# Kernel tuning notes

Hardware: AMD Instinct MI355X
Metric: run time of the kernel (lower is better)

The kernel has to match this reference:

```python
import jax, jax.numpy as jnp
import numpy as np

B, LAT, HID = 256, 20, 128
G, BIN = 25000, 25       # original_dim, bin_size
C = 7                    # max_cp + 1 copy-number states
GB = G // BIN            # rho head output dim


def setup_inputs() -> dict:
    key = jax.random.key(0)
    ks = jax.random.split(key, 16)
    s = 0.01  # TruncatedNormal(stddev=0.01) init
    return {
        "z": jax.random.normal(ks[0], (B, LAT), jnp.float32),
        "w0": jax.random.normal(ks[1], (LAT, HID), jnp.float32) * s,
        "b0": jnp.zeros((HID,), jnp.float32),
        "g0": jnp.ones((HID,), jnp.float32),
        "be0": jnp.zeros((HID,), jnp.float32),
        "m0": jax.random.normal(ks[2], (HID,), jnp.float32) * 0.1,
        "v0": jax.random.uniform(ks[3], (HID,), jnp.float32, 0.5, 1.5),
        "w1": jax.random.normal(ks[4], (HID, HID), jnp.float32) * s,
        "b1": jnp.zeros((HID,), jnp.float32),
        "g1": jnp.ones((HID,), jnp.float32),
        "be1": jnp.zeros((HID,), jnp.float32),
        "m1": jax.random.normal(ks[5], (HID,), jnp.float32) * 0.1,
        "v1": jax.random.uniform(ks[6], (HID,), jnp.float32, 0.5, 1.5),
        "wr": jax.random.normal(ks[7], (HID, G), jnp.float32) * s,
        "br": jnp.zeros((G,), jnp.float32),
        "wd": jax.random.normal(ks[8], (HID, G), jnp.float32) * s,
        "bd": jnp.zeros((G,), jnp.float32),
        "wrho": jax.random.normal(ks[9], (C, HID, GB), jnp.float32) * s,
        "brho": jnp.zeros((C, GB), jnp.float32),
        "ws": jax.random.normal(ks[10], (G,), jnp.float32) * 0.05,
        "bs": jax.random.normal(ks[11], (G,), jnp.float32) * 0.05,
    }


def reference(z, w0, b0, g0, be0, m0, v0, w1, b1, g1, be1, m1, v1,
              wr, br, wd, bd, wrho, brho, ws, bs):
    BN_EPS = 1e-3
    EPS = 1e-20
    TEMP = 0.1

    def bn(x, gamma, beta, mean, var):
        # inference-mode BatchNormalization(momentum=0.01, epsilon=0.001)
        return (x - mean) * jax.lax.rsqrt(var + BN_EPS) * gamma + beta

    # FullyConnLayer x2: Dense -> BN -> ReLU
    x = jax.nn.relu(bn(z @ w0 + b0, g0, be0, m0, v0))
    x = jax.nn.relu(bn(x @ w1 + b1, g1, be1, m1, v1))

    theta = jnp.exp(x @ wr + br)        # [B, G]
    pi_drop = x @ wd + bd               # [B, G]

    # max_cp+1 rho Dense heads fused into a single batched GEMM -> [C, B, GB]
    rho = jnp.einsum('bh,cho->cbo', x, wrho) + brho[:, None, :]
    rho = jax.nn.softmax(rho, axis=0)   # softmax over copy-number states

    # GumbelSoftmaxSampling: stack(axis=1) -> [B, C, GB]
    rho_b = jnp.transpose(rho, (1, 0, 2))
    gene_rho = jnp.repeat(rho_b, BIN, axis=-1)        # [B, C, G]
    pi = jnp.transpose(gene_rho, (0, 2, 1))           # [B, G, C]

    u = jax.random.uniform(jax.random.key(42), pi.shape, jnp.float32)
    gnoise = -jnp.log(-jnp.log(u + EPS) + EPS)
    y = jax.nn.softmax((jnp.log(pi + EPS) + gnoise) / TEMP, axis=-1)
    y_hard = (y == jnp.max(y, axis=-1, keepdims=True)).astype(jnp.float32)
    y = jax.lax.stop_gradient(y_hard - y) + y         # straight-through

    # multiply by copy-number index matrix and reduce -> expected/sampled copy
    cvals = jnp.arange(C, dtype=jnp.float32)
    sample = jnp.sum(y * cvals, axis=-1)              # [B, G]

    # ScaleLayer: sigmoid(x * w + b)
    mu = jax.nn.sigmoid(sample * ws + bs)             # [B, G]
    return (mu, theta, pi_drop, sample, pi)
```

## Files before the change

### kernel.cpp

```cpp
#include <hip/hip_runtime.h>

#define B 256
#define LAT 20
#define HID 128
#define G 25000
#define GB 1000
#define NC 7

typedef __attribute__((ext_vector_type(8))) short short8;
typedef __attribute__((ext_vector_type(4))) float f32x4;

__device__ __forceinline__ unsigned short f2bf(float f) {
  unsigned int u = __float_as_uint(f);
  u += 0x7fffu + ((u >> 16) & 1u);
  return (unsigned short)(u >> 16);
}

__device__ __forceinline__ unsigned int threefry_xor(unsigned int idx) {
  unsigned int x0 = 0u;
  unsigned int x1 = idx + 42u;
#define TF_R(r) { x0 += x1; x1 = (x1 << r) | (x1 >> (32 - r)); x1 ^= x0; }
  TF_R(13) TF_R(15) TF_R(26) TF_R(6)
  x0 += 42u;          x1 += 0x1BD11BF1u;
  TF_R(17) TF_R(29) TF_R(16) TF_R(24)
  x0 += 0x1BD11BF0u;  x1 += 2u;
  TF_R(13) TF_R(15) TF_R(26) TF_R(6)
   x1 += 45u;
  TF_R(17) TF_R(29) TF_R(16) TF_R(24)
  x0 += 42u;          x1 += 0x1BD11BF4u;
  TF_R(13) TF_R(15) TF_R(26) TF_R(6)
  x0 += 0x1BD11BF0u;  x1 += 5u;
#undef TF_R
  return x0 ^ x1;
}

__global__ void k_mlp(const float* __restrict__ z,  const float* __restrict__ w0,
                      const float* __restrict__ b0, const float* __restrict__ g0,
                      const float* __restrict__ be0, const float* __restrict__ m0,
                      const float* __restrict__ v0,
                      const float* __restrict__ w1, const float* __restrict__ b1,
                      const float* __restrict__ g1, const float* __restrict__ be1,
                      const float* __restrict__ m1, const float* __restrict__ v1,
                      double* __restrict__ x64, unsigned short* __restrict__ x_bf) {
  __shared__ double xs[HID];
  const int b = blockIdx.x, h = threadIdx.x;
  double acc = (double)b0[h];
  for (int k = 0; k < LAT; ++k)
    acc += (double)z[b * LAT + k] * (double)w0[k * HID + h];
  double y = (acc - (double)m0[h]) * (1.0 / sqrt((double)v0[h] + 1e-3)) * (double)g0[h]
             + (double)be0[h];
  y = y > 0.0 ? y : 0.0;
  xs[h] = y;
  __syncthreads();
  double a1 = (double)b1[h];
  for (int k = 0; k < HID; ++k)
    a1 += xs[k] * (double)w1[k * HID + h];
  double y1 = (a1 - (double)m1[h]) * (1.0 / sqrt((double)v1[h] + 1e-3)) * (double)g1[h]
              + (double)be1[h];
  y1 = y1 > 0.0 ? y1 : 0.0;
  x64[h * B + b] = y1;
  x_bf[b * HID + h] = f2bf((float)y1);
}

__global__ void k_trans(const float* __restrict__ wr, const float* __restrict__ wd,
                        unsigned short* __restrict__ wrT, unsigned short* __restrict__ wdT) {
  __shared__ float t[64][65];
  const float* src = blockIdx.z ? wd : wr;
  unsigned short* dst = blockIdx.z ? wdT : wrT;
  const int g0 = blockIdx.x * 64, h0 = blockIdx.y * 64;
#pragma unroll
  for (int i = 0; i < 16; ++i) {
    int f = i * 256 + threadIdx.x;
    int hl = f >> 6, gl = f & 63;
    int g = g0 + gl;
    t[hl][gl] = (g < G) ? src[(h0 + hl) * G + g] : 0.f;
  }
  __syncthreads();
#pragma unroll
  for (int i = 0; i < 16; ++i) {
    int f = i * 256 + threadIdx.x;
    int gl = f >> 6, hl = f & 63;
    int g = g0 + gl;
    if (g < G) dst[(size_t)g * HID + h0 + hl] = f2bf(t[hl][gl]);
  }
}

__global__ __launch_bounds__(256) void k_rho(const double* __restrict__ x64,
                      const float* __restrict__ wrho, const float* __restrict__ brho,
                      float* __restrict__ pi32, float* __restrict__ lp32,
                      double* __restrict__ lp64) {
  __shared__ float wl[NC * HID * 4];
  const int o0 = blockIdx.x * 4, bB = blockIdx.y * 64;
  for (int i = threadIdx.x; i < NC * HID * 4; i += 256) {
    int ol = i & 3, rest = i >> 2;
    int c = rest >> 7, h = rest & 127;
    wl[i] = wrho[(c * HID + h) * GB + o0 + ol];
  }
  __syncthreads();
  const int lane = threadIdx.x & 63, ol = threadIdx.x >> 6;
  const int b = bB + lane, o = o0 + ol;
  double acc[NC];
#pragma unroll
  for (int c = 0; c < NC; ++c) acc[c] = (double)brho[c * GB + o];
  for (int h = 0; h < HID; ++h) {
    double xv = x64[h * B + b];
#pragma unroll
    for (int c = 0; c < NC; ++c)
      acc[c] += xv * (double)wl[(c * HID + h) * 4 + ol];
  }
  double m = acc[0];
#pragma unroll
  for (int c = 1; c < NC; ++c) m = fmax(m, acc[c]);
  double e[NC], s = 0.0;
#pragma unroll
  for (int c = 0; c < NC; ++c) { e[c] = exp(acc[c] - m); s += e[c]; }
  const size_t base = (size_t)o * (NC * B) + b;
#pragma unroll
  for (int c = 0; c < NC; ++c) {
    double pi = e[c] / s;
    double lp = log(pi + 1e-20);
    pi32[base + c * B] = (float)pi;
    lp32[base + c * B] = (float)lp;
    lp64[base + c * B] = lp;
  }
}

__global__ __launch_bounds__(256) void k_main(
    const unsigned short* __restrict__ x_bf,
    const unsigned short* __restrict__ wrT, const unsigned short* __restrict__ wdT,
    const float* __restrict__ br, const float* __restrict__ bd,
    const float* __restrict__ wsc, const float* __restrict__ bsc,
    const float* __restrict__ pi32, const float* __restrict__ lp32,
    const double* __restrict__ lp64, float* __restrict__ out) {
  __shared__ float s_lp[3 * NC * 128];
  __shared__ float s_pi[3 * NC * 128];
  const int tid = threadIdx.x;
  const int o_base = (blockIdx.x * 32) / 25;
  const int bB = blockIdx.y * 128;

  for (int i = tid; i < 3 * NC * 128; i += 256) {
    int ol = i / (NC * 128);
    int r = i - ol * (NC * 128);
    int c = r >> 7, bl = r & 127;
    int oo = o_base + ol; if (oo > GB - 1) oo = GB - 1;
    size_t src = (size_t)oo * (NC * B) + c * B + bB + bl;
    s_lp[i] = lp32[src];
    s_pi[i] = pi32[src];
  }

  const int wv = tid >> 6, lane = tid & 63;
  const int n = lane & 15, quad = lane >> 4;
  const int gt = wv & 1;
  const int btbase = blockIdx.y * 8 + (wv >> 1) * 4;
  const int g = blockIdx.x * 32 + gt * 16 + n;
  const bool gvalid = g < G;
  const int gcl = gvalid ? g : G - 1;
  const float brv = br[gcl], bdv = bd[gcl], wsv = wsc[gcl], bsv = bsc[gcl];
  const int o = gcl / 25;
  const int o_local = o - o_base;
  const double* lqb = lp64 + (size_t)o * (NC * B);

  short8 fr[4], fd[4];
  {
    const short8* p1 = (const short8*)(wrT + (size_t)gcl * HID + quad * 8);
    const short8* p2 = (const short8*)(wdT + (size_t)gcl * HID + quad * 8);
#pragma unroll
    for (int ks = 0; ks < 4; ++ks) { fr[ks] = p1[ks * 4]; fd[ks] = p2[ks * 4]; }
  }
  __syncthreads();

  for (int bti = 0; bti < 4; ++bti) {
    const int bt = btbase + bti;
    const short8* xp = (const short8*)(x_bf + (size_t)(bt * 16 + n) * HID + quad * 8);
    f32x4 accr = {0.f, 0.f, 0.f, 0.f}, accd = {0.f, 0.f, 0.f, 0.f};
#pragma unroll
    for (int ks = 0; ks < 4; ++ks) {
      short8 fa = xp[ks * 4];
      accr = __builtin_amdgcn_mfma_f32_16x16x32_bf16(fa, fr[ks], accr, 0, 0, 0);
      accd = __builtin_amdgcn_mfma_f32_16x16x32_bf16(fa, fd[ks], accd, 0, 0, 0);
    }
#pragma unroll
    for (int i = 0; i < 4; ++i) {
      const int b = bt * 16 + quad * 4 + i;
      const int b_local = (wv >> 1) * 64 + bti * 16 + quad * 4 + i;
      const float th = __expf(accr[i] + brv);
      const float pd = accd[i] + bdv;
      const float* lpp = s_lp + o_local * (NC * 128) + b_local;
      unsigned int bits[NC];
      const unsigned int idx0 = (unsigned int)b * 175000u + (unsigned int)g * 7u;
      float best = -3.4e38f, sec = -3.4e38f; int arg = 0;
#pragma unroll
      for (int c = 0; c < NC; ++c) {
        unsigned int bb = threefry_xor(idx0 + (unsigned int)c);
        bits[c] = bb;
        float uf = __uint_as_float((bb >> 9) | 0x3f800000u) - 1.0f;
        float v1m = 1.0f - uf;
        float ln_nat = -__logf(uf + 1e-20f);
        float ln_ser = v1m * (1.0f + v1m * (0.5f + 0.33333334f * v1m));
        float l1 = (v1m < 0.001953125f) ? ln_ser : ln_nat;
        float gn = -__logf(l1);
        float mv = lpp[c * 128] + gn;
        if (mv > best) { sec = best; best = mv; arg = c; }
        else if (mv > sec) sec = mv;
      }
      int s = arg;
      if (best - sec < 3e-4f) {
        double lv[NC], bestd = -1e300;
#pragma unroll
        for (int c = 0; c < NC; ++c) {
          float uf = __uint_as_float((bits[c] >> 9) | 0x3f800000u) - 1.0f;
          double gn = -log(-log((double)uf + 1e-20) + 1e-20);
          lv[c] = lqb[c * B + b] + gn;
          bestd = fmax(bestd, lv[c]);
        }
        s = 0;
#pragma unroll
        for (int c = 0; c < NC; ++c) if (lv[c] == bestd) s += c;
      }
      if (gvalid) {
        const float smp = (float)s;
        const float mu = __builtin_amdgcn_rcpf(1.f + __expf(-(smp * wsv + bsv)));
        const size_t og = (size_t)b * G + g;
        out[og] = mu;
        out[6400000 + og] = th;
        out[12800000 + og] = pd;
        out[19200000 + og] = smp;
        const float* pip = s_pi + o_local * (NC * 128) + b_local;
        const size_t pbo = 25600000 + og * 7;
#pragma unroll
        for (int c = 0; c < NC; ++c) out[pbo + c] = pip[c * 128];
      }
    }
  }
}

extern "C" void kernel_launch(void* const* d_in, const int* in_sizes, int n_in,
                              void* d_out, int out_size, void* d_ws, size_t ws_size,
                              hipStream_t stream) {
  const float* z   = (const float*)d_in[0];
  const float* w0  = (const float*)d_in[1];
  const float* b0  = (const float*)d_in[2];
  const float* g0  = (const float*)d_in[3];
  const float* be0 = (const float*)d_in[4];
  const float* m0  = (const float*)d_in[5];
  const float* v0  = (const float*)d_in[6];
  const float* w1  = (const float*)d_in[7];
  const float* b1  = (const float*)d_in[8];
  const float* g1  = (const float*)d_in[9];
  const float* be1 = (const float*)d_in[10];
  const float* m1  = (const float*)d_in[11];
  const float* v1  = (const float*)d_in[12];
  const float* wr  = (const float*)d_in[13];
  const float* br  = (const float*)d_in[14];
  const float* wd  = (const float*)d_in[15];
  const float* bd  = (const float*)d_in[16];
  const float* wrho= (const float*)d_in[17];
  const float* brho= (const float*)d_in[18];
  const float* wsc = (const float*)d_in[19];
  const float* bsc = (const float*)d_in[20];

  char* ws = (char*)d_ws;
  unsigned short* x_bf = (unsigned short*)(ws);
  double* x64          = (double*)(ws + 65536);
  unsigned short* wrT  = (unsigned short*)(ws + 327680);
  unsigned short* wdT  = (unsigned short*)(ws + 6727680);
  float* pi32          = (float*)(ws + 13127680);
  float* lp32          = (float*)(ws + 20295680);
  double* lp64         = (double*)(ws + 27463680);
  float* out = (float*)d_out;

  k_mlp<<<dim3(256), dim3(128), 0, stream>>>(z, w0, b0, g0, be0, m0, v0,
                                             w1, b1, g1, be1, m1, v1, x64, x_bf);
  k_trans<<<dim3(391, 2, 2), dim3(256), 0, stream>>>(wr, wd, wrT, wdT);
  k_rho<<<dim3(250, 4), dim3(256), 0, stream>>>(x64, wrho, brho, pi32, lp32, lp64);
  k_main<<<dim3(782, 2), dim3(256), 0, stream>>>(x_bf, wrT, wdT, br, bd, wsc, bsc,
                                                 pi32, lp32, lp64, out);
}
```

Before: 522.3 us.

## Defer near-tie double-precision Gumbel argmax fixups to a separate compacted kernel

Near-tie samples are no longer recomputed in double precision inside the main kernel. The main kernel appends their (b,g) indices to a global list via an atomic counter, and a small follow-up kernel recomputes and overwrites mu and sample for those entries. This removes divergent fp64 work and register pressure (bits array, unrolled loop) from the hot kernel. It also vectorizes the pi stores. In exchange it adds atomics, an extra launch, and a capped list that could overflow.

```diff
diff --git a/kernel.cpp b/kernel.cpp
--- a/kernel.cpp
+++ b/kernel.cpp
@@ -6,9 +6,12 @@
 #define G 25000
 #define GB 1000
 #define NC 7
+#define FIXCAP (1u << 20)
 
 typedef __attribute__((ext_vector_type(8))) short short8;
 typedef __attribute__((ext_vector_type(4))) float f32x4;
+typedef float v4fa __attribute__((vector_size(16), aligned(4)));
+typedef float v2fa __attribute__((vector_size(8), aligned(4)));
 
 __device__ __forceinline__ unsigned short f2bf(float f) {
   unsigned int u = __float_as_uint(f);
@@ -41,7 +44,10 @@
                       const float* __restrict__ w1, const float* __restrict__ b1,
                       const float* __restrict__ g1, const float* __restrict__ be1,
                       const float* __restrict__ m1, const float* __restrict__ v1,
-                      double* __restrict__ x64, unsigned short* __restrict__ x_bf) {
+                      double* __restrict__ x64, unsigned short* __restrict__ x_bf,
+                      unsigned int* __restrict__ fix_cnt) {
+  if (blockIdx.x == 0 && threadIdx.x == 0)
+    __hip_atomic_store(fix_cnt, 0u, __ATOMIC_RELAXED, __HIP_MEMORY_SCOPE_AGENT);
   __shared__ double xs[HID];
   const int b = blockIdx.x, h = threadIdx.x;
   double acc = (double)b0[h];
@@ -131,7 +137,8 @@
     const float* __restrict__ br, const float* __restrict__ bd,
     const float* __restrict__ wsc, const float* __restrict__ bsc,
     const float* __restrict__ pi32, const float* __restrict__ lp32,
-    const double* __restrict__ lp64, float* __restrict__ out) {
+    unsigned int* __restrict__ fix_cnt, unsigned int* __restrict__ fix_list,
+    float* __restrict__ out) {
   __shared__ float s_lp[3 * NC * 128];
   __shared__ float s_pi[3 * NC * 128];
   const int tid = threadIdx.x;
@@ -158,7 +165,6 @@
   const float brv = br[gcl], bdv = bd[gcl], wsv = wsc[gcl], bsv = bsc[gcl];
   const int o = gcl / 25;
   const int o_local = o - o_base;
-  const double* lqb = lp64 + (size_t)o * (NC * B);
 
   short8 fr[4], fd[4];
   {
@@ -186,13 +192,11 @@
       const float th = __expf(accr[i] + brv);
       const float pd = accd[i] + bdv;
       const float* lpp = s_lp + o_local * (NC * 128) + b_local;
-      unsigned int bits[NC];
       const unsigned int idx0 = (unsigned int)b * 175000u + (unsigned int)g * 7u;
       float best = -3.4e38f, sec = -3.4e38f; int arg = 0;
-#pragma unroll
+#pragma unroll 1
       for (int c = 0; c < NC; ++c) {
         unsigned int bb = threefry_xor(idx0 + (unsigned int)c);
-        bits[c] = bb;
         float uf = __uint_as_float((bb >> 9) | 0x3f800000u) - 1.0f;
         float v1m = 1.0f - uf;
         float ln_nat = -__logf(uf + 1e-20f);
@@ -200,25 +204,17 @@
         float l1 = (v1m < 0.001953125f) ? ln_ser : ln_nat;
         float gn = -__logf(l1);
         float mv = lpp[c * 128] + gn;
-        if (mv > best) { sec = best; best = mv; arg = c; }
-        else if (mv > sec) sec = mv;
-      }
-      int s = arg;
-      if (best - sec < 3e-4f) {
-        double lv[NC], bestd = -1e300;
-#pragma unroll
-        for (int c = 0; c < NC; ++c) {
-          float uf = __uint_as_float((bits[c] >> 9) | 0x3f800000u) - 1.0f;
-          double gn = -log(-log((double)uf + 1e-20) + 1e-20);
-          lv[c] = lqb[c * B + b] + gn;
-          bestd = fmax(bestd, lv[c]);
-        }
-        s = 0;
-#pragma unroll
-        for (int c = 0; c < NC; ++c) if (lv[c] == bestd) s += c;
+        bool gtb = mv > best;
+        sec = gtb ? best : (mv > sec ? mv : sec);
+        best = gtb ? mv : best;
+        arg = gtb ? c : arg;
       }
       if (gvalid) {
-        const float smp = (float)s;
+        if (best - sec < 3e-4f) {
+          unsigned int idx = atomicAdd(fix_cnt, 1u);
+          if (idx < FIXCAP) fix_list[idx] = ((unsigned int)b << 15) | (unsigned int)g;
+        }
+        const float smp = (float)arg;
         const float mu = __builtin_amdgcn_rcpf(1.f + __expf(-(smp * wsv + bsv)));
         const size_t og = (size_t)b * G + g;
         out[og] = mu;
@@ -227,10 +223,46 @@
         out[19200000 + og] = smp;
         const float* pip = s_pi + o_local * (NC * 128) + b_local;
         const size_t pbo = 25600000 + og * 7;
-#pragma unroll
-        for (int c = 0; c < NC; ++c) out[pbo + c] = pip[c * 128];
+        v4fa p4 = {pip[0], pip[128], pip[256], pip[384]};
+        v2fa p2 = {pip[512], pip[640]};
+        *(v4fa*)(out + pbo) = p4;
+        *(v2fa*)(out + pbo + 4) = p2;
+        out[pbo + 6] = pip[768];
       }
     }
+  }
+}
+
+__global__ void k_fix(const double* __restrict__ lp64,
+                      const float* __restrict__ wsc, const float* __restrict__ bsc,
+                      const unsigned int* __restrict__ fix_cnt,
+                      const unsigned int* __restrict__ fix_list,
+                      float* __restrict__ out) {
+  unsigned int nn = fix_cnt[0];
+  if (nn > FIXCAP) nn = FIXCAP;
+  for (unsigned int i = blockIdx.x * 256 + threadIdx.x; i < nn; i += gridDim.x * 256) {
+    unsigned int bg = fix_list[i];
+    int b = bg >> 15, g = bg & 32767;
+    int o = g / 25;
+    const double* lq = lp64 + (size_t)o * (NC * B) + b;
+    const unsigned int idx0 = (unsigned int)b * 175000u + (unsigned int)g * 7u;
+    double lv[NC], bestd = -1e300;
+#pragma unroll
+    for (int c = 0; c < NC; ++c) {
+      unsigned int bb = threefry_xor(idx0 + (unsigned int)c);
+      float uf = __uint_as_float((bb >> 9) | 0x3f800000u) - 1.0f;
+      double gn = -log(-log((double)uf + 1e-20) + 1e-20);
+      lv[c] = lq[c * B] + gn;
+      bestd = fmax(bestd, lv[c]);
+    }
+    int s = 0;
+#pragma unroll
+    for (int c = 0; c < NC; ++c) if (lv[c] == bestd) s += c;
+    const float smp = (float)s;
+    const float mu = __builtin_amdgcn_rcpf(1.f + __expf(-(smp * wsc[g] + bsc[g])));
+    const size_t og = (size_t)b * G + g;
+    out[og] = mu;
+    out[19200000 + og] = smp;
   }
 }
 
@@ -267,12 +299,15 @@
   float* pi32          = (float*)(ws + 13127680);
   float* lp32          = (float*)(ws + 20295680);
   double* lp64         = (double*)(ws + 27463680);
+  unsigned int* fix_cnt  = (unsigned int*)(ws + 48 * 1024 * 1024);
+  unsigned int* fix_list = (unsigned int*)(ws + 48 * 1024 * 1024 + 16);
   float* out = (float*)d_out;
 
   k_mlp<<<dim3(256), dim3(128), 0, stream>>>(z, w0, b0, g0, be0, m0, v0,
-                                             w1, b1, g1, be1, m1, v1, x64, x_bf);
+                                             w1, b1, g1, be1, m1, v1, x64, x_bf, fix_cnt);
   k_trans<<<dim3(391, 2, 2), dim3(256), 0, stream>>>(wr, wd, wrT, wdT);
   k_rho<<<dim3(250, 4), dim3(256), 0, stream>>>(x64, wrho, brho, pi32, lp32, lp64);
   k_main<<<dim3(782, 2), dim3(256), 0, stream>>>(x_bf, wrT, wdT, br, bd, wsc, bsc,
-                                                 pi32, lp32, lp64, out);
-}
+                                                 pi32, lp32, fix_cnt, fix_list, out);
+  k_fix<<<dim3(96), dim3(256), 0, stream>>>(lp64, wsc, bsc, fix_cnt, fix_list, out);
+}
```

Result: slower. 551.8 us (+5.6%).
